# Optimization experiments

Measured on AMD Instinct MI355X. Metric: run time of the kernel, lower is better.

The kernel has to match this reference:

```python
import jax, jax.numpy as jnp
import numpy as np

N_NODES = 50000
N_EDGES = 800000
D = 128
AVG_D_LOG = 2.833  # log(avg_degree + 1)
EPS = 1e-5


def setup_inputs() -> dict:
    key = jax.random.key(0)
    ks = jax.random.split(key, 8)
    h = jax.random.normal(ks[0], (N_NODES, D), dtype=jnp.float32)
    e = jax.random.normal(ks[1], (N_EDGES, D), dtype=jnp.float32)
    snorm_n = jax.random.uniform(ks[2], (N_NODES, 1), dtype=jnp.float32)
    src = jax.random.randint(ks[3], (N_EDGES,), 0, N_NODES)
    dst = jax.random.randint(ks[4], (N_EDGES,), 0, N_NODES)
    W_pre = jax.random.normal(ks[5], (3 * D, D), dtype=jnp.float32) * 0.05
    b_pre = jnp.zeros((D,), dtype=jnp.float32)
    W_post = jax.random.normal(ks[6], (13 * D, D), dtype=jnp.float32) * 0.05
    b_post = jnp.zeros((D,), dtype=jnp.float32)
    return {"h": h, "e": e, "snorm_n": snorm_n, "src": src, "dst": dst,
            "W_pre": W_pre, "b_pre": b_pre, "W_post": W_post, "b_post": b_post}


def _pna_forward(h, e, snorm_n, src, dst, W_pre, b_pre, W_post, b_post):
    N = h.shape[0]
    # pretrans_edges: gather endpoint features + edge features, single Linear (pretrans_layers=1)
    z2 = jnp.concatenate([h[src], h[dst], e], axis=1)           # [E, 3D]
    m = z2 @ W_pre + b_pre                                        # [E, D] per-edge message

    # reduce: multi-aggregator mailbox reduce over dst (ragged neighborhoods)
    deg = jax.ops.segment_sum(jnp.ones((m.shape[0],), m.dtype), dst, num_segments=N)  # [N]
    deg_safe = jnp.maximum(deg, 1.0)[:, None]
    s = jax.ops.segment_sum(m, dst, num_segments=N)
    s2 = jax.ops.segment_sum(m * m, dst, num_segments=N)
    mean = s / deg_safe
    var = jax.nn.relu(s2 / deg_safe - mean * mean)
    std = jnp.sqrt(var + EPS)
    mx = jax.ops.segment_max(m, dst, num_segments=N)
    mn = jax.ops.segment_min(m, dst, num_segments=N)
    has = (deg > 0)[:, None]
    mx = jnp.where(has, mx, 0.0)
    mn = jnp.where(has, mn, 0.0)
    agg = jnp.concatenate([mean, mx, mn, std], axis=1)            # [N, 4D]

    # scalers: identity, amplification, attenuation
    log_d = jnp.log(deg[:, None] + 1.0)
    log_d_safe = jnp.log(deg_safe + 1.0)
    amp = agg * (log_d / AVG_D_LOG)
    att = agg * (AVG_D_LOG / log_d_safe)
    scaled = jnp.concatenate([agg, amp, att], axis=1)             # [N, 12D]
    scaled = jnp.where(has, scaled, 0.0)                          # DGL zero-fills zero-degree nodes

    # posttrans: cat original h, single Linear (posttrans_layers=1), then graph_norm
    h_cat = jnp.concatenate([h, scaled], axis=1)                  # [N, 13D]
    out = h_cat @ W_post + b_post                                 # [N, D]
    out = out * snorm_n                                           # graph_norm; dropout p=0 is identity
    return out


def reference(h, e, snorm_n, src, dst, W_pre, b_pre, W_post, b_post):
    return _pna_forward(h, e, snorm_n, src, dst, W_pre, b_pre, W_post, b_post)
```

## Files before the change

kernel.cpp:

```cpp
#include <hip/hip_runtime.h>
#include <math.h>

#define NNODES 50000
#define NEDGES 800000
#define AVGDLOG 2.833f
#define EPSF 1e-5f
#define TPB_E 16

typedef __attribute__((ext_vector_type(8))) short short8;
typedef __attribute__((ext_vector_type(4))) float f32x4;

__device__ __forceinline__ unsigned f2bf(float x) {
    unsigned u = __float_as_uint(x);
    return (u + 0x7FFFu + ((u >> 16) & 1u)) >> 16;
}
__device__ __forceinline__ float bf2f(unsigned lo16) {
    return __uint_as_float(lo16 << 16);
}
__device__ __forceinline__ void up8(uint4 v, float* f) {
    f[0] = bf2f(v.x & 0xffffu); f[1] = bf2f(v.x >> 16);
    f[2] = bf2f(v.y & 0xffffu); f[3] = bf2f(v.y >> 16);
    f[4] = bf2f(v.z & 0xffffu); f[5] = bf2f(v.z >> 16);
    f[6] = bf2f(v.w & 0xffffu); f[7] = bf2f(v.w >> 16);
}
__device__ __forceinline__ uint4 pk8(const float* f) {
    uint4 v;
    v.x = f2bf(f[0]) | (f2bf(f[1]) << 16);
    v.y = f2bf(f[2]) | (f2bf(f[3]) << 16);
    v.z = f2bf(f[4]) | (f2bf(f[5]) << 16);
    v.w = f2bf(f[6]) | (f2bf(f[7]) << 16);
    return v;
}

__global__ void k_zero(unsigned* __restrict__ deg) {
    int i = blockIdx.x * 256 + threadIdx.x;
    if (i < NNODES) deg[i] = 0u;
}
__global__ void k_count(const int* __restrict__ dst, unsigned* __restrict__ deg) {
    int i = blockIdx.x * 256 + threadIdx.x;
    if (i < NEDGES) atomicAdd(&deg[dst[i]], 1u);
}
__global__ __launch_bounds__(1024) void k_scan(const unsigned* __restrict__ deg,
                                               int* __restrict__ base, int* __restrict__ cursor) {
    __shared__ int ps[1024];
    const int t = threadIdx.x;
    const int lo = t * 52;
    int s = 0;
    if (lo + 52 <= NNODES) {
        const int4* dp = (const int4*)(deg + lo);
#pragma unroll
        for (int i = 0; i < 13; ++i) { int4 v = dp[i]; s += v.x + v.y + v.z + v.w; }
    } else {
        for (int i = lo; i < NNODES; ++i) s += (int)deg[i];
    }
    ps[t] = s;
    __syncthreads();
    for (int off = 1; off < 1024; off <<= 1) {
        int v = (t >= off) ? ps[t - off] : 0;
        __syncthreads();
        ps[t] += v;
        __syncthreads();
    }
    int run = (t > 0) ? ps[t - 1] : 0;
    if (lo + 52 <= NNODES) {
        const int4* dp = (const int4*)(deg + lo);
        int4* bp = (int4*)(base + lo);
        int4* cp = (int4*)(cursor + lo);
#pragma unroll
        for (int i = 0; i < 13; ++i) {
            int4 v = dp[i]; int4 b;
            b.x = run; run += v.x; b.y = run; run += v.y;
            b.z = run; run += v.z; b.w = run; run += v.w;
            bp[i] = b; cp[i] = b;
        }
    } else {
        for (int i = lo; i < NNODES; ++i) { base[i] = run; cursor[i] = run; run += (int)deg[i]; }
    }
    if (t == 1023) base[NNODES] = run;
}
__global__ void k_scatter(const int* __restrict__ dst, const int* __restrict__ src,
                          int* __restrict__ cursor, int* __restrict__ sorted,
                          int* __restrict__ ssrc) {
    int i = blockIdx.x * 256 + threadIdx.x;
    if (i < NEDGES) {
        int d = dst[i];
        int slot = atomicAdd(&cursor[d], 1);
        sorted[slot] = i;
        ssrc[slot] = src[i];
    }
}

__global__ void k_convW(const float* __restrict__ Wpre, const float* __restrict__ Wpost,
                        unsigned short* __restrict__ W3t, unsigned short* __restrict__ W12t,
                        unsigned short* __restrict__ Bhat) {
    int i = blockIdx.x * 256 + threadIdx.x;
    if (i < 128 * 128) {
        int n = i & 127, k = i >> 7;
        W3t[n * 128 + k] = (unsigned short)f2bf(Wpre[(256 + k) * 128 + n]);
    }
    if (i < 256 * 128) {
        int n = i >> 7, k = i & 127;
        float v = (n < 128) ? Wpre[k * 128 + n] : Wpre[(128 + k) * 128 + (n - 128)];
        W12t[n * 128 + k] = (unsigned short)f2bf(v);
    }
    if (i < 640 * 384) {
        int kc = i / (384 * 32);
        int rem = i % (384 * 32);
        int n = rem >> 5, kk = rem & 31;
        int k = kc * 32 + kk, c = n & 127, g = n >> 7;
        float v;
        if (g == 0) v = Wpost[k * 128 + c];
        else if (g == 1) v = (k < 128) ? 0.f : Wpost[(512 + k) * 128 + c];
        else v = (k < 128) ? 0.f : Wpost[(1024 + k) * 128 + c];
        Bhat[i] = (unsigned short)f2bf(v);
    }
}

__global__ __launch_bounds__(256) void k_p12(const float* __restrict__ h,
                                             const unsigned short* __restrict__ W12t,
                                             unsigned short* __restrict__ P1,
                                             unsigned short* __restrict__ P2,
                                             unsigned short* __restrict__ Abuf) {
    __shared__ __align__(16) unsigned short As[64 * 128];
    __shared__ __align__(16) unsigned short Bs[256 * 128];
    const int t = threadIdx.x;
    const size_t row0 = (size_t)blockIdx.x * 64;
#pragma unroll
    for (int j = 0; j < 16; ++j) {
        int idx = t + 256 * j;
        int n = idx >> 4, q = idx & 15;
        uint4 wv = *(const uint4*)(W12t + n * 128 + q * 8);
        *(uint4*)((char*)Bs + n * 256 + ((q * 16) ^ ((n & 7) << 4))) = wv;
    }
#pragma unroll
    for (int j = 0; j < 8; ++j) {
        int idx = t + 256 * j;
        int r = idx >> 5, q = idx & 31;
        size_t row = row0 + r;
        uint2 p = {0u, 0u};
        if (row < NNODES) {
            float4 z = ((const float4*)h)[row * 32 + q];
            p.x = f2bf(z.x) | (f2bf(z.y) << 16);
            p.y = f2bf(z.z) | (f2bf(z.w) << 16);
            *(uint2*)(Abuf + row * 640 + q * 4) = p;
        }
        *(uint2*)((char*)As + r * 256 + ((q * 8) ^ ((r & 7) << 4))) = p;
    }
    __syncthreads();
    const int w = t >> 6, lane = t & 63, lrow = lane & 15, lkb = lane >> 4;
    f32x4 acc[16];
#pragma unroll
    for (int i = 0; i < 16; ++i) acc[i] = (f32x4){0.f, 0.f, 0.f, 0.f};
    const char* Abase = (const char*)As + (w * 16 + lrow) * 256;
    const unsigned aswz = (unsigned)(((w * 16 + lrow) & 7) << 4);
#pragma unroll
    for (int kk = 0; kk < 4; ++kk) {
        int kbyte = (kk * 32 + lkb * 8) * 2;
        short8 af = *(const short8*)(Abase + (kbyte ^ aswz));
#pragma unroll
        for (int nt = 0; nt < 16; ++nt) {
            int n = nt * 16 + lrow;
            short8 bf = *(const short8*)((const char*)Bs + n * 256 + (kbyte ^ ((n & 7) << 4)));
            acc[nt] = __builtin_amdgcn_mfma_f32_16x16x32_bf16(af, bf, acc[nt], 0, 0, 0);
        }
    }
#pragma unroll
    for (int half = 0; half < 2; ++half) {
        __syncthreads();
#pragma unroll
        for (int nt = 0; nt < 8; ++nt) {
            int c = nt * 16 + lrow;
#pragma unroll
            for (int i = 0; i < 4; ++i) {
                int lr = w * 16 + lkb * 4 + i;
                *(unsigned short*)((char*)As + lr * 256 + ((c * 2) ^ ((lr & 7) << 4))) =
                    (unsigned short)f2bf(acc[half * 8 + nt][i]);
            }
        }
        __syncthreads();
        unsigned short* dstP = half ? P2 : P1;
#pragma unroll
        for (int j = 0; j < 4; ++j) {
            int idx = t + 256 * j;
            int r = idx >> 4, q = idx & 15;
            size_t row = row0 + r;
            if (row < NNODES) {
                uint4 v = *(const uint4*)((const char*)As + r * 256 + ((q * 16) ^ ((r & 7) << 4)));
                *(uint4*)(dstP + row * 128 + q * 8) = v;
            }
        }
    }
}

__global__ __launch_bounds__(256) void k_gemm_e(const float* __restrict__ e,
                                                const int* __restrict__ sorted,
                                                const unsigned short* __restrict__ W3t,
                                                const float* __restrict__ bpre,
                                                unsigned short* __restrict__ G) {
    __shared__ __align__(16) unsigned short Bs[128 * 128];
    __shared__ __align__(16) unsigned short As[2][64 * 128];
    __shared__ int Seid[TPB_E * 64];
    const int t = threadIdx.x;
    const int tile0 = blockIdx.x * TPB_E;
    const int ntiles = min(TPB_E, 12500 - tile0);

    for (int j = t; j < TPB_E * 64; j += 256) {
        int slot = tile0 * 64 + j;
        Seid[j] = (slot < NEDGES) ? sorted[slot] : 0;
    }
    __syncthreads();

    const int q = t & 31, r5 = t >> 5;
    auto loadE = [&](int ti, float4* ra) {
#pragma unroll
        for (int j = 0; j < 8; ++j) {
            int r = r5 + 8 * j;
            int eid = Seid[ti * 64 + r];
            ra[j] = ((const float4*)e)[(size_t)eid * 32 + q];
        }
    };
    auto storeA = [&](int buf, const float4* ra) {
#pragma unroll
        for (int j = 0; j < 8; ++j) {
            int r = r5 + 8 * j;
            uint2 pv;
            pv.x = f2bf(ra[j].x) | (f2bf(ra[j].y) << 16);
            pv.y = f2bf(ra[j].z) | (f2bf(ra[j].w) << 16);
            *(uint2*)((char*)As[buf] + r * 256 + ((q * 8) ^ ((r & 7) << 4))) = pv;
        }
    };

    float4 ra[8];
    loadE(0, ra);
#pragma unroll
    for (int j = 0; j < 8; ++j) {
        int idx = t + 256 * j;
        int n = idx >> 4, qq = idx & 15;
        uint4 wv = *(const uint4*)(W3t + n * 128 + qq * 8);
        *(uint4*)((char*)Bs + n * 256 + ((qq * 16) ^ ((n & 7) << 4))) = wv;
    }
    storeA(0, ra);
    if (ntiles > 1) loadE(1, ra);
    __syncthreads();

    const int w = t >> 6, lane = t & 63, lrow = lane & 15, lkb = lane >> 4;
    float bpf[8];
#pragma unroll
    for (int nt = 0; nt < 8; ++nt) bpf[nt] = bpre[nt * 16 + lrow];

    for (int ti = 0; ti < ntiles; ++ti) {
        const int c = ti & 1;
        f32x4 acc[8];
#pragma unroll
        for (int i = 0; i < 8; ++i) acc[i] = (f32x4){0.f, 0.f, 0.f, 0.f};
        const char* Ab = (const char*)As[c] + (w * 16 + lrow) * 256;
        const unsigned aswz = (unsigned)(((w * 16 + lrow) & 7) << 4);
#pragma unroll
        for (int kk = 0; kk < 4; ++kk) {
            int kbyte = (kk * 32 + lkb * 8) * 2;
            short8 af = *(const short8*)(Ab + (kbyte ^ aswz));
#pragma unroll
            for (int nt = 0; nt < 8; ++nt) {
                int n = nt * 16 + lrow;
                short8 bf = *(const short8*)((const char*)Bs + n * 256 + (kbyte ^ ((n & 7) << 4)));
                acc[nt] = __builtin_amdgcn_mfma_f32_16x16x32_bf16(af, bf, acc[nt], 0, 0, 0);
            }
        }
        __syncthreads();
#pragma unroll
        for (int nt = 0; nt < 8; ++nt) {
            int cc = nt * 16 + lrow;
#pragma unroll
            for (int i = 0; i < 4; ++i) {
                int lr = w * 16 + lkb * 4 + i;
                *(unsigned short*)((char*)As[c] + lr * 256 + ((cc * 2) ^ ((lr & 7) << 4))) =
                    (unsigned short)f2bf(acc[nt][i] + bpf[nt]);
            }
        }
        if (ti + 1 < ntiles) {
            storeA(c ^ 1, ra);
            if (ti + 2 < ntiles) loadE(ti + 2, ra);
        }
        __syncthreads();
        const size_t row0 = (size_t)(tile0 + ti) * 64;
#pragma unroll
        for (int j = 0; j < 4; ++j) {
            int idx = t + 256 * j;
            int r = idx >> 4, qq = idx & 15;
            uint4 v = *(const uint4*)((const char*)As[c] + r * 256 + ((qq * 16) ^ ((r & 7) << 4)));
            *(uint4*)(G + (row0 + r) * 128 + qq * 8) = v;
        }
    }
}

__global__ __launch_bounds__(256) void k_reduce(const unsigned short* __restrict__ G,
                                                const unsigned short* __restrict__ P1,
                                                const unsigned short* __restrict__ P2,
                                                const int* __restrict__ basep,
                                                const int* __restrict__ ssrc,
                                                unsigned short* __restrict__ Abuf) {
    const int t = threadIdx.x;
    const int n = blockIdx.x * 4 + (t >> 6);
    const int lane = t & 63, lq = lane >> 4, lc = lane & 15;
    int b0 = basep[n], b1 = basep[n + 1];
    int dg = b1 - b0;
    float s[8], q2[8], mx[8], mn[8];
#pragma unroll
    for (int j = 0; j < 8; ++j) { s[j] = 0.f; q2[j] = 0.f; mx[j] = -3.4e38f; mn[j] = 3.4e38f; }
    if (dg > 0) {
        float p2f[8];
        up8(*(const uint4*)(P2 + (size_t)n * 128 + lc * 8), p2f);
        for (int sl = b0 + lq; sl < b1; sl += 4) {
            int es = ssrc[sl];
            float gf[8], p1f[8];
            up8(*(const uint4*)(G + (size_t)sl * 128 + lc * 8), gf);
            up8(*(const uint4*)(P1 + (size_t)es * 128 + lc * 8), p1f);
#pragma unroll
            for (int j = 0; j < 8; ++j) {
                float m = gf[j] + p1f[j] + p2f[j];
                s[j] += m; q2[j] += m * m;
                mx[j] = fmaxf(mx[j], m); mn[j] = fminf(mn[j], m);
            }
        }
    }
#pragma unroll
    for (int off = 16; off <= 32; off <<= 1) {
#pragma unroll
        for (int j = 0; j < 8; ++j) {
            s[j] += __shfl_xor(s[j], off);
            q2[j] += __shfl_xor(q2[j], off);
            mx[j] = fmaxf(mx[j], __shfl_xor(mx[j], off));
            mn[j] = fminf(mn[j], __shfl_xor(mn[j], off));
        }
    }
    if (lane < 16) {
        float mean[8], sd[8], X[8], N[8];
        if (dg > 0) {
            float ds = (float)dg;
#pragma unroll
            for (int j = 0; j < 8; ++j) {
                mean[j] = s[j] / ds;
                float v = fmaxf(q2[j] / ds - mean[j] * mean[j], 0.f);
                sd[j] = sqrtf(v + EPSF);
                X[j] = mx[j]; N[j] = mn[j];
            }
        } else {
#pragma unroll
            for (int j = 0; j < 8; ++j) { mean[j] = 0.f; sd[j] = 0.f; X[j] = 0.f; N[j] = 0.f; }
        }
        unsigned short* row = Abuf + (size_t)n * 640 + 128 + lc * 8;
        *(uint4*)(row) = pk8(mean);
        *(uint4*)(row + 128) = pk8(X);
        *(uint4*)(row + 256) = pk8(N);
        *(uint4*)(row + 384) = pk8(sd);
    }
}

__global__ __launch_bounds__(256) void k_gemm_post(const unsigned short* __restrict__ Abuf,
                                                   const unsigned short* __restrict__ Bhat,
                                                   const float* __restrict__ bpost,
                                                   const float* __restrict__ snorm,
                                                   const int* __restrict__ basep,
                                                   float* __restrict__ out) {
    __shared__ __align__(16) unsigned short As[2][64 * 32];
    __shared__ __align__(16) unsigned short Bs[2][384 * 32];
    __shared__ float sAmp[64], sAtt[64], sSn[64], sBp[128];
    const int t = threadIdx.x;
    const size_t row0 = (size_t)blockIdx.x * 64;
    if (t < 64) {
        size_t nn = row0 + t;
        float a = 0.f, b = 0.f, sn = 0.f;
        if (nn < NNODES) {
            int dgi = basep[nn + 1] - basep[nn];
            a = logf((float)dgi + 1.f) * (1.f / AVGDLOG);
            b = AVGDLOG / logf(fmaxf((float)dgi, 1.f) + 1.f);
            sn = snorm[nn];
        }
        sAmp[t] = a; sAtt[t] = b; sSn[t] = sn;
    }
    if (t < 128) sBp[t] = bpost[t];
    const int arow = t >> 2, ak4 = t & 3;
    auto loadA = [&](int kc, uint4& ra) {
        ra = (uint4){0u, 0u, 0u, 0u};
        if (row0 + arow < NNODES)
            ra = *(const uint4*)(Abuf + (row0 + arow) * 640 + kc * 32 + ak4 * 8);
    };
    auto loadB = [&](int kc, uint4* rb) {
#pragma unroll
        for (int j = 0; j < 6; ++j) {
            int idx = t + 256 * j;
            int n = idx >> 2, k4 = idx & 3;
            rb[j] = *(const uint4*)(Bhat + ((size_t)kc * 384 + n) * 32 + k4 * 8);
        }
    };
    auto storeLDS = [&](int buf, const uint4& ra, const uint4* rb) {
        *(uint4*)((char*)As[buf] + arow * 64 + ((ak4 * 16) ^ (((arow >> 1) & 3) << 4))) = ra;
#pragma unroll
        for (int j = 0; j < 6; ++j) {
            int idx = t + 256 * j;
            int n = idx >> 2, k4 = idx & 3;
            *(uint4*)((char*)Bs[buf] + n * 64 + ((k4 * 16) ^ (((n >> 1) & 3) << 4))) = rb[j];
        }
    };
    const int w = t >> 6;
    const int lane = t & 63, lrow = lane & 15, lkb = lane >> 4;
    f32x4 acc[4][6];
#pragma unroll
    for (int a = 0; a < 4; ++a)
#pragma unroll
        for (int b = 0; b < 6; ++b) acc[a][b] = (f32x4){0.f, 0.f, 0.f, 0.f};

    uint4 ra, rb[6];
    loadA(0, ra); loadB(0, rb);
    storeLDS(0, ra, rb);
    int cur = 0;
    for (int kc = 0; kc < 20; ++kc) {
        if (kc < 19) { loadA(kc + 1, ra); loadB(kc + 1, rb); }
        __syncthreads();
        short8 af[4];
#pragma unroll
        for (int mi = 0; mi < 4; ++mi) {
            int r = mi * 16 + lrow;
            af[mi] = *(const short8*)((const char*)As[cur] + r * 64 + ((lkb * 16) ^ (((r >> 1) & 3) << 4)));
        }
        short8 bfv[6];
#pragma unroll
        for (int g = 0; g < 3; ++g)
#pragma unroll
            for (int j = 0; j < 2; ++j) {
                int nn = g * 128 + w * 32 + j * 16 + lrow;
                bfv[g * 2 + j] = *(const short8*)((const char*)Bs[cur] + nn * 64 + ((lkb * 16) ^ (((nn >> 1) & 3) << 4)));
            }
#pragma unroll
        for (int mi = 0; mi < 4; ++mi)
#pragma unroll
            for (int f = 0; f < 6; ++f)
                acc[mi][f] = __builtin_amdgcn_mfma_f32_16x16x32_bf16(af[mi], bfv[f], acc[mi][f], 0, 0, 0);
        if (kc < 19) storeLDS(cur ^ 1, ra, rb);
        cur ^= 1;
    }
#pragma unroll
    for (int mi = 0; mi < 4; ++mi)
#pragma unroll
        for (int j = 0; j < 2; ++j)
#pragma unroll
            for (int i = 0; i < 4; ++i) {
                int r = mi * 16 + lkb * 4 + i;
                size_t grow = row0 + r;
                if (grow < NNODES) {
                    int c = w * 32 + j * 16 + lrow;
                    float v = acc[mi][j][i] + sAmp[r] * acc[mi][2 + j][i] + sAtt[r] * acc[mi][4 + j][i] + sBp[c];
                    out[grow * 128 + c] = v * sSn[r];
                }
            }
}

extern "C" void kernel_launch(void* const* d_in, const int* in_sizes, int n_in,
                              void* d_out, int out_size, void* d_ws, size_t ws_size,
                              hipStream_t stream) {
    const float* h = (const float*)d_in[0];
    const float* e = (const float*)d_in[1];
    const float* snorm = (const float*)d_in[2];
    const int* src = (const int*)d_in[3];
    const int* dst = (const int*)d_in[4];
    const float* Wpre = (const float*)d_in[5];
    const float* bpre = (const float*)d_in[6];
    const float* Wpost = (const float*)d_in[7];
    const float* bpost = (const float*)d_in[8];
    float* out = (float*)d_out;

    char* p = (char*)d_ws;
    auto alloc = [&](size_t bytes) { char* r = p; p += (bytes + 255) & ~(size_t)255; return r; };
    unsigned short* P1 = (unsigned short*)alloc((size_t)NNODES * 128 * 2);
    unsigned short* P2 = (unsigned short*)alloc((size_t)NNODES * 128 * 2);
    unsigned short* Abuf = (unsigned short*)alloc((size_t)NNODES * 640 * 2);
    unsigned short* G = (unsigned short*)alloc((size_t)NEDGES * 128 * 2);
    unsigned short* W3t = (unsigned short*)alloc(128 * 128 * 2);
    unsigned short* W12t = (unsigned short*)alloc(256 * 128 * 2);
    unsigned short* Bhat = (unsigned short*)alloc((size_t)640 * 384 * 2);
    unsigned* deg = (unsigned*)alloc((size_t)NNODES * 4);
    int* basep = (int*)alloc((size_t)(NNODES + 1) * 4);
    int* cursor = (int*)alloc((size_t)NNODES * 4);
    int* sorted = (int*)alloc((size_t)NEDGES * 4);
    int* ssrc = (int*)alloc((size_t)NEDGES * 4);

    k_zero<<<(NNODES + 255) / 256, 256, 0, stream>>>(deg);
    k_count<<<(NEDGES + 255) / 256, 256, 0, stream>>>(dst, deg);
    k_scan<<<1, 1024, 0, stream>>>(deg, basep, cursor);
    k_scatter<<<(NEDGES + 255) / 256, 256, 0, stream>>>(dst, src, cursor, sorted, ssrc);
    k_convW<<<(640 * 384 + 255) / 256, 256, 0, stream>>>(Wpre, Wpost, W3t, W12t, Bhat);
    k_p12<<<(NNODES + 63) / 64, 256, 0, stream>>>(h, W12t, P1, P2, Abuf);
    k_gemm_e<<<(12500 + TPB_E - 1) / TPB_E, 256, 0, stream>>>(e, sorted, W3t, bpre, G);
    k_reduce<<<NNODES / 4, 256, 0, stream>>>(G, P1, P2, basep, ssrc, Abuf);
    k_gemm_post<<<(NNODES + 63) / 64, 256, 0, stream>>>(Abuf, Bhat, bpost, snorm, basep, out);
}
```

Before: 539.6 us.

## Drop LDS staging in post GEMM; each wave reads B fragments directly from global

```diff
diff --git a/kernel.cpp b/kernel.cpp
--- a/kernel.cpp
+++ b/kernel.cpp
@@ -5,7 +5,7 @@
 #define NEDGES 800000
 #define AVGDLOG 2.833f
 #define EPSF 1e-5f
-#define TPB_E 16
+#define TPB_E 8
 
 typedef __attribute__((ext_vector_type(8))) short short8;
 typedef __attribute__((ext_vector_type(4))) float f32x4;
@@ -362,97 +362,45 @@
                                                    const float* __restrict__ snorm,
                                                    const int* __restrict__ basep,
                                                    float* __restrict__ out) {
-    __shared__ __align__(16) unsigned short As[2][64 * 32];
-    __shared__ __align__(16) unsigned short Bs[2][384 * 32];
-    __shared__ float sAmp[64], sAtt[64], sSn[64], sBp[128];
     const int t = threadIdx.x;
-    const size_t row0 = (size_t)blockIdx.x * 64;
-    if (t < 64) {
-        size_t nn = row0 + t;
-        float a = 0.f, b = 0.f, sn = 0.f;
-        if (nn < NNODES) {
-            int dgi = basep[nn + 1] - basep[nn];
-            a = logf((float)dgi + 1.f) * (1.f / AVGDLOG);
-            b = AVGDLOG / logf(fmaxf((float)dgi, 1.f) + 1.f);
-            sn = snorm[nn];
-        }
-        sAmp[t] = a; sAtt[t] = b; sSn[t] = sn;
-    }
-    if (t < 128) sBp[t] = bpost[t];
-    const int arow = t >> 2, ak4 = t & 3;
-    auto loadA = [&](int kc, uint4& ra) {
-        ra = (uint4){0u, 0u, 0u, 0u};
-        if (row0 + arow < NNODES)
-            ra = *(const uint4*)(Abuf + (row0 + arow) * 640 + kc * 32 + ak4 * 8);
-    };
-    auto loadB = [&](int kc, uint4* rb) {
-#pragma unroll
-        for (int j = 0; j < 6; ++j) {
-            int idx = t + 256 * j;
-            int n = idx >> 2, k4 = idx & 3;
-            rb[j] = *(const uint4*)(Bhat + ((size_t)kc * 384 + n) * 32 + k4 * 8);
-        }
-    };
-    auto storeLDS = [&](int buf, const uint4& ra, const uint4* rb) {
-        *(uint4*)((char*)As[buf] + arow * 64 + ((ak4 * 16) ^ (((arow >> 1) & 3) << 4))) = ra;
-#pragma unroll
-        for (int j = 0; j < 6; ++j) {
-            int idx = t + 256 * j;
-            int n = idx >> 2, k4 = idx & 3;
-            *(uint4*)((char*)Bs[buf] + n * 64 + ((k4 * 16) ^ (((n >> 1) & 3) << 4))) = rb[j];
-        }
-    };
-    const int w = t >> 6;
-    const int lane = t & 63, lrow = lane & 15, lkb = lane >> 4;
-    f32x4 acc[4][6];
-#pragma unroll
-    for (int a = 0; a < 4; ++a)
-#pragma unroll
-        for (int b = 0; b < 6; ++b) acc[a][b] = (f32x4){0.f, 0.f, 0.f, 0.f};
-
-    uint4 ra, rb[6];
-    loadA(0, ra); loadB(0, rb);
-    storeLDS(0, ra, rb);
-    int cur = 0;
+    const int w = t >> 6, lane = t & 63, lrow = lane & 15, lkb = lane >> 4;
+    const int grow = blockIdx.x * 64 + w * 16 + lrow;
+    const bool rv = grow < NNODES;
+    f32x4 acc[24];
+#pragma unroll
+    for (int f = 0; f < 24; ++f) acc[f] = (f32x4){0.f, 0.f, 0.f, 0.f};
+    const unsigned short* ap = Abuf + (size_t)(rv ? grow : 0) * 640 + lkb * 8;
+    const unsigned short* bb = Bhat + lrow * 32 + lkb * 8;
     for (int kc = 0; kc < 20; ++kc) {
-        if (kc < 19) { loadA(kc + 1, ra); loadB(kc + 1, rb); }
-        __syncthreads();
-        short8 af[4];
-#pragma unroll
-        for (int mi = 0; mi < 4; ++mi) {
-            int r = mi * 16 + lrow;
-            af[mi] = *(const short8*)((const char*)As[cur] + r * 64 + ((lkb * 16) ^ (((r >> 1) & 3) << 4)));
-        }
-        short8 bfv[6];
-#pragma unroll
-        for (int g = 0; g < 3; ++g)
-#pragma unroll
-            for (int j = 0; j < 2; ++j) {
-                int nn = g * 128 + w * 32 + j * 16 + lrow;
-                bfv[g * 2 + j] = *(const short8*)((const char*)Bs[cur] + nn * 64 + ((lkb * 16) ^ (((nn >> 1) & 3) << 4)));
-            }
-#pragma unroll
-        for (int mi = 0; mi < 4; ++mi)
-#pragma unroll
-            for (int f = 0; f < 6; ++f)
-                acc[mi][f] = __builtin_amdgcn_mfma_f32_16x16x32_bf16(af[mi], bfv[f], acc[mi][f], 0, 0, 0);
-        if (kc < 19) storeLDS(cur ^ 1, ra, rb);
-        cur ^= 1;
-    }
-#pragma unroll
-    for (int mi = 0; mi < 4; ++mi)
-#pragma unroll
-        for (int j = 0; j < 2; ++j)
-#pragma unroll
-            for (int i = 0; i < 4; ++i) {
-                int r = mi * 16 + lkb * 4 + i;
-                size_t grow = row0 + r;
-                if (grow < NNODES) {
-                    int c = w * 32 + j * 16 + lrow;
-                    float v = acc[mi][j][i] + sAmp[r] * acc[mi][2 + j][i] + sAtt[r] * acc[mi][4 + j][i] + sBp[c];
-                    out[grow * 128 + c] = v * sSn[r];
-                }
-            }
+        short8 af = *(const short8*)(ap + kc * 32);
+        if (!rv) af = (short8){0, 0, 0, 0, 0, 0, 0, 0};
+        const unsigned short* bk = bb + (size_t)kc * (384 * 32);
+#pragma unroll
+        for (int f = 0; f < 24; ++f) {
+            short8 bf = *(const short8*)(bk + f * 512);
+            acc[f] = __builtin_amdgcn_mfma_f32_16x16x32_bf16(af, bf, acc[f], 0, 0, 0);
+        }
+    }
+    const int orow0 = blockIdx.x * 64 + w * 16 + lkb * 4;
+    float bpc[8];
+#pragma unroll
+    for (int j = 0; j < 8; ++j) bpc[j] = bpost[j * 16 + lrow];
+#pragma unroll
+    for (int i = 0; i < 4; ++i) {
+        int r = orow0 + i;
+        if (r < NNODES) {
+            int dgi = basep[r + 1] - basep[r];
+            float a = logf((float)dgi + 1.f) * (1.f / AVGDLOG);
+            float b = AVGDLOG / logf(fmaxf((float)dgi, 1.f) + 1.f);
+            float sn = snorm[r];
+#pragma unroll
+            for (int j = 0; j < 8; ++j) {
+                int c = j * 16 + lrow;
+                float v = acc[j][i] + a * acc[8 + j][i] + b * acc[16 + j][i] + bpc[j];
+                out[(size_t)r * 128 + c] = v * sn;
+            }
+        }
+    }
 }
 
 extern "C" void kernel_launch(void* const* d_in, const int* in_sizes, int n_in,
```

Result: slower. 558.0 us (+3.4%).
